# Kernel tuning notes

Hardware: AMD Instinct MI355X
Metric: run time of the kernel (lower is better)

Reference implementation:

```python
import jax, jax.numpy as jnp
import numpy as np

H = 64  # hidden width hard-coded in Agent body


def setup_inputs() -> dict:
    key = jax.random.key(0)
    ks = jax.random.split(key, 10)
    T, B, OBS, A = 1024, 512, 128, 18
    x = jax.random.normal(ks[0], (T, B, OBS), dtype=jnp.float32)
    mask = jax.random.bernoulli(ks[1], 0.01, (T, B))
    initial_carry = jnp.zeros((B, H), dtype=jnp.float32)
    s = lambda k, sh: (jax.random.normal(k, sh, dtype=jnp.float32) * 0.05)
    W1 = s(ks[2], (OBS, H)); b1 = jnp.zeros((H,), jnp.float32)
    Wi = s(ks[3], (H, 3 * H)); bi = jnp.zeros((3 * H,), jnp.float32)
    Wh = s(ks[4], (H, 3 * H)); bhn = jnp.zeros((H,), jnp.float32)
    W2 = s(ks[5], (H, H)); b2 = jnp.zeros((H,), jnp.float32)
    Wl = s(ks[6], (H, A)); bl = jnp.zeros((A,), jnp.float32)
    Wv = s(ks[7], (H, 1)); bv = jnp.zeros((1,), jnp.float32)
    return dict(x=x, mask=mask, initial_carry=initial_carry,
                W1=W1, b1=b1, Wi=Wi, bi=bi, Wh=Wh, bhn=bhn,
                W2=W2, b2=b2, Wl=Wl, bl=bl, Wv=Wv, bv=bv)


def _gru(h, z_t, Wi, bi, Wh, bhn):
    # flax nn.GRUCell math
    gi = z_t @ Wi + bi            # [B, 3H]
    gh = h @ Wh                   # [B, 3H]
    ir, iz, inn = jnp.split(gi, 3, axis=-1)
    hr, hz, hn = jnp.split(gh, 3, axis=-1)
    r = jax.nn.sigmoid(ir + hr)
    u = jax.nn.sigmoid(iz + hz)
    n = jnp.tanh(inn + r * (hn + bhn))
    return (1.0 - u) * n + u * h


def reference(x, mask, initial_carry, W1, b1, Wi, bi, Wh, bhn, W2, b2, Wl, bl, Wv, bv):
    # stem: Dense(64) + relu, applied to all timesteps at once
    z = jax.nn.relu(x @ W1 + b1)                  # [T, B, H]
    m = mask[..., None]                           # [T, B, 1]

    def step(h, inp):
        z_t, m_t = inp
        # masked reset of the carry at episode boundaries
        h = jnp.where(m_t, initial_carry, h)
        h = _gru(h, z_t, Wi, bi, Wh, bhn)
        return h, h

    h_final, ys = jax.lax.scan(step, initial_carry, (z, m))  # ys: [T, B, H]

    y = jax.nn.relu(ys @ W2 + b2)                 # [T, B, H]
    logits = y @ Wl + bl                          # [T, B, A]
    value = y @ Wv + bv                           # [T, B, 1]
    return h_final, logits.squeeze(), value.squeeze(-1)
```

## Files before the change

kernel.cpp:

```cpp
#include <hip/hip_runtime.h>
#include <stdint.h>

#define TT  1024
#define BB  512
#define OBS 128
#define HH  64
#define AA  18
#define RT  (TT*BB)
#define OFF_L ((size_t)BB*HH)
#define OFF_V (OFF_L + (size_t)TT*BB*AA)

#define GI_ELEMS ((size_t)RT*192)
#define WS_NEED  ((GI_ELEMS + (size_t)RT*HH)*4)

typedef __attribute__((ext_vector_type(8))) short bf16x8;
typedef __attribute__((ext_vector_type(4))) float f32x4;
typedef __attribute__((ext_vector_type(4))) unsigned int u32x4;

__device__ __forceinline__ float fast_rcp(float x){ return __builtin_amdgcn_rcpf(x); }
__device__ __forceinline__ float sigm(float x){ return fast_rcp(1.f + __expf(-x)); }
__device__ __forceinline__ float tanh_(float x){ return 1.f - 2.f*fast_rcp(1.f + __expf(2.f*x)); }

__device__ __forceinline__ unsigned bf16_rne(float f){
    unsigned u = __float_as_uint(f);
    return (u + 0x7FFFu + ((u>>16)&1u)) >> 16;
}
__device__ __forceinline__ unsigned pk_bf16(float lo, float hi){
    unsigned d;
    asm("v_cvt_pk_bf16_f32 %0, %1, %2" : "=v"(d) : "v"(lo), "v"(hi));
    return d;
}

__global__ void detect_mask(const uint32_t* __restrict__ m, uint32_t* __restrict__ flag)
{
    const int n_words = (TT * BB) / 4;
    uint32_t acc = 0;
    for (int i = blockIdx.x * blockDim.x + threadIdx.x; i < n_words;
         i += gridDim.x * blockDim.x)
        acc |= (m[i] > 1u) ? 1u : 0u;
    if (acc) flag[0] = 1u;
}

#define P1_BLOCKS 1024
#define ZSTR 70

__global__ __launch_bounds__(256, 2)
void stem_gi(const float* __restrict__ x,
             const float* __restrict__ W1, const float* __restrict__ b1,
             const float* __restrict__ Wi, const float* __restrict__ bi,
             float* __restrict__ gi)
{
    const int tid = threadIdx.x, w = tid >> 6, l = tid & 63;
    const int a = l & 15, q = l >> 4;

    __shared__ float z_s[4][16*ZSTR];
    float* zw = &z_s[w][0];

    bf16x8 W1f[4][4];
    #pragma unroll
    for (int nt = 0; nt < 4; ++nt)
        #pragma unroll
        for (int kf = 0; kf < 4; ++kf) {
            u32x4 pk;
            #pragma unroll
            for (int j2 = 0; j2 < 4; ++j2) {
                const int k0 = kf*32 + q*8 + 2*j2;
                pk[j2] = bf16_rne(W1[(size_t)k0*HH + nt*16 + a])
                       | (bf16_rne(W1[(size_t)(k0+1)*HH + nt*16 + a]) << 16);
            }
            W1f[nt][kf] = __builtin_bit_cast(bf16x8, pk);
        }
    float b1v[4];
    #pragma unroll
    for (int nt = 0; nt < 4; ++nt) b1v[nt] = b1[nt*16 + a];

    bf16x8 Wif[12][2];
    #pragma unroll
    for (int tau = 0; tau < 12; ++tau)
        #pragma unroll
        for (int kf = 0; kf < 2; ++kf) {
            u32x4 pk;
            #pragma unroll
            for (int j2 = 0; j2 < 4; ++j2) {
                const int k0 = kf*32 + q*8 + 2*j2;
                pk[j2] = bf16_rne(Wi[(size_t)k0*192 + tau*16 + a])
                       | (bf16_rne(Wi[(size_t)(k0+1)*192 + tau*16 + a]) << 16);
            }
            Wif[tau][kf] = __builtin_bit_cast(bf16x8, pk);
        }
    float biv[12];
    #pragma unroll
    for (int tau = 0; tau < 12; ++tau) biv[tau] = bi[tau*16 + a];

    for (int it = 0; it < 8; ++it) {
        const size_t grp  = (size_t)blockIdx.x*32 + it*4 + w;
        const float* xr   = x + (grp*16 + a)*OBS;

        float4 xv[8];
        #pragma unroll
        for (int kf = 0; kf < 4; ++kf) {
            xv[2*kf]   = *(const float4*)(xr + kf*32 + q*8);
            xv[2*kf+1] = *(const float4*)(xr + kf*32 + q*8 + 4);
        }
        bf16x8 Af[4];
        #pragma unroll
        for (int kf = 0; kf < 4; ++kf) {
            u32x4 pk;
            pk[0] = pk_bf16(xv[2*kf].x,   xv[2*kf].y);
            pk[1] = pk_bf16(xv[2*kf].z,   xv[2*kf].w);
            pk[2] = pk_bf16(xv[2*kf+1].x, xv[2*kf+1].y);
            pk[3] = pk_bf16(xv[2*kf+1].z, xv[2*kf+1].w);
            Af[kf] = __builtin_bit_cast(bf16x8, pk);
        }

        #pragma unroll
        for (int nt = 0; nt < 4; ++nt) {
            f32x4 D = {b1v[nt], b1v[nt], b1v[nt], b1v[nt]};
            #pragma unroll
            for (int kf = 0; kf < 4; ++kf)
                D = __builtin_amdgcn_mfma_f32_16x16x32_bf16(Af[kf], W1f[nt][kf], D, 0,0,0);
            #pragma unroll
            for (int e = 0; e < 4; ++e)
                zw[(q*4 + e)*ZSTR + nt*16 + a] = fmaxf(D[e], 0.f);
        }
        bf16x8 Az[2];
        #pragma unroll
        for (int s = 0; s < 2; ++s) {
            u32x4 pk;
            #pragma unroll
            for (int j2 = 0; j2 < 4; ++j2) {
                const float2 f = *(const float2*)(zw + a*ZSTR + s*32 + q*8 + 2*j2);
                pk[j2] = pk_bf16(f.x, f.y);
            }
            Az[s] = __builtin_bit_cast(bf16x8, pk);
        }

        float* gb = gi + grp*12*256 + l*4;
        #pragma unroll
        for (int tau = 0; tau < 12; ++tau) {
            f32x4 D = {biv[tau], biv[tau], biv[tau], biv[tau]};
            D = __builtin_amdgcn_mfma_f32_16x16x32_bf16(Az[0], Wif[tau][0], D, 0,0,0);
            D = __builtin_amdgcn_mfma_f32_16x16x32_bf16(Az[1], Wif[tau][1], D, 0,0,0);
            *(f32x4*)(gb + (size_t)tau*256) = D;
        }
    }
}

#define HSTR 70

__global__ __launch_bounds__(256)
void recur5(const float* __restrict__ gip,
            const void* __restrict__ mask_raw,
            const uint32_t* __restrict__ mflag,
            const float* __restrict__ ic,
            const float* __restrict__ Wh,
            const float* __restrict__ bhn,
            float* __restrict__ ys,
            float* __restrict__ out)
{
    const int blk = blockIdx.x;
    const int tid = threadIdx.x;
    const int w   = tid >> 6;
    const int l   = tid & 63;
    const int a   = l & 15;
    const int q   = l >> 4;
    const int dw  = w*16 + a;

    __shared__ unsigned short h16[2][16][HSTR];
    __shared__ uint32_t mbits[TT];

    if (mflag[0] != 0) {
        const uint8_t* m8 = (const uint8_t*)mask_raw;
        for (int t0 = w*4; t0 < TT; t0 += 16) {
            const int tt = t0 + q;
            const uint64_t bal = __ballot(m8[(size_t)tt*BB + blk*16 + a] != 0);
            if (l < 4) mbits[t0 + l] = (uint32_t)((bal >> (16*l)) & 0xFFFFu);
        }
    } else {
        const int32_t* m32 = (const int32_t*)mask_raw;
        for (int t0 = w*4; t0 < TT; t0 += 16) {
            const int tt = t0 + q;
            const uint64_t bal = __ballot(m32[(size_t)tt*BB + blk*16 + a] != 0);
            if (l < 4) mbits[t0 + l] = (uint32_t)((bal >> (16*l)) & 0xFFFFu);
        }
    }
    for (int i = tid; i < 16*64; i += 256) {
        const int c = i >> 6, d = i & 63;
        h16[0][c][d] = (unsigned short)bf16_rne(ic[(blk*16 + c)*HH + d]);
    }

    bf16x8 Bf[3][2];
    #pragma unroll
    for (int g = 0; g < 3; ++g) {
        const int colb = g*64 + dw;
        #pragma unroll
        for (int s = 0; s < 2; ++s) {
            u32x4 pk;
            #pragma unroll
            for (int j2 = 0; j2 < 4; ++j2) {
                const int k0 = s*32 + q*8 + j2*2;
                pk[j2] = bf16_rne(Wh[(size_t)k0*192 + colb])
                       | (bf16_rne(Wh[(size_t)(k0+1)*192 + colb]) << 16);
            }
            Bf[g][s] = __builtin_bit_cast(bf16x8, pk);
        }
    }
    u32x4 icA[2];
    #pragma unroll
    for (int s = 0; s < 2; ++s) {
        #pragma unroll
        for (int j2 = 0; j2 < 4; ++j2) {
            const int d0 = s*32 + q*8 + j2*2;
            icA[s][j2] = bf16_rne(ic[(blk*16 + a)*HH + d0])
                       | (bf16_rne(ic[(blk*16 + a)*HH + d0 + 1]) << 16);
        }
    }
    float ic_c[4], h_reg[4];
    #pragma unroll
    for (int e = 0; e < 4; ++e) {
        ic_c[e]  = ic[(blk*16 + q*4 + e)*HH + dw];
        h_reg[e] = ic_c[e];
    }
    const float bhnv = bhn[dw];
    const f32x4 Cn = {bhnv, bhnv, bhnv, bhnv};

    __syncthreads();

    #define GSTRIDE ((size_t)32*12*256)
    const float* gbase = gip + (size_t)blk*12*256 + l*4;
    f32x4 bufA[3], bufB[3];
    #pragma unroll
    for (int g = 0; g < 3; ++g) {
        bufA[g] = *(const f32x4*)(gbase + 0*GSTRIDE + (size_t)(g*4 + w)*256);
        bufB[g] = *(const f32x4*)(gbase + 1*GSTRIDE + (size_t)(g*4 + w)*256);
    }

    auto step = [&](int t, f32x4* cur) {
        const int p = t & 1;
        const uint32_t mb = mbits[t];
        const bool mA = (mb >> a) & 1;
        const uint32_t* hrow = (const uint32_t*)&h16[p][a][0];
        u32x4 Apk[2];
        #pragma unroll
        for (int s = 0; s < 2; ++s) {
            #pragma unroll
            for (int j2 = 0; j2 < 4; ++j2) {
                const uint32_t pkv = hrow[s*16 + q*4 + j2];
                Apk[s][j2] = mA ? icA[s][j2] : pkv;
            }
        }
        const bf16x8 A0 = __builtin_bit_cast(bf16x8, Apk[0]);
        const bf16x8 A1 = __builtin_bit_cast(bf16x8, Apk[1]);
        f32x4 Dr = __builtin_amdgcn_mfma_f32_16x16x32_bf16(A0, Bf[0][0], cur[0], 0,0,0);
        Dr       = __builtin_amdgcn_mfma_f32_16x16x32_bf16(A1, Bf[0][1], Dr,     0,0,0);
        f32x4 Dz = __builtin_amdgcn_mfma_f32_16x16x32_bf16(A0, Bf[1][0], cur[1], 0,0,0);
        Dz       = __builtin_amdgcn_mfma_f32_16x16x32_bf16(A1, Bf[1][1], Dz,     0,0,0);
        f32x4 Dn = __builtin_amdgcn_mfma_f32_16x16x32_bf16(A0, Bf[2][0], Cn,     0,0,0);
        Dn       = __builtin_amdgcn_mfma_f32_16x16x32_bf16(A1, Bf[2][1], Dn,     0,0,0);
        const f32x4 gin = cur[2];
        const int tp = (t + 2 < TT) ? (t + 2) : (TT - 1);
        #pragma unroll
        for (int g = 0; g < 3; ++g)
            cur[g] = *(const f32x4*)(gbase + (size_t)tp*GSTRIDE + (size_t)(g*4 + w)*256);
        float* ysp = ys + ((size_t)t*BB + blk*16 + q*4)*HH + dw;
        #pragma unroll
        for (int e = 0; e < 4; ++e) {
            const bool me   = (mb >> (q*4 + e)) & 1;
            const float he  = me ? ic_c[e] : h_reg[e];
            const float r   = sigm(Dr[e]);
            const float u   = sigm(Dz[e]);
            const float n   = tanh_(fmaf(r, Dn[e], gin[e]));
            const float hn  = fmaf(u, he - n, n);
            h_reg[e] = hn;
            h16[p ^ 1][q*4 + e][dw] = (unsigned short)bf16_rne(hn);
            ysp[(size_t)e*HH] = hn;
        }
        asm volatile("s_waitcnt lgkmcnt(0)" ::: "memory");
        __builtin_amdgcn_s_barrier();
        __builtin_amdgcn_sched_barrier(0);
    };

    for (int t = 0; t < TT; t += 2) {
        step(t,     bufA);
        step(t + 1, bufB);
    }
    #pragma unroll
    for (int e = 0; e < 4; ++e)
        out[(size_t)(blk*16 + q*4 + e)*HH + dw] = h_reg[e];
    #undef GSTRIDE
}

#define P3_BLOCKS 1024
#define P3_RPW (RT/(P3_BLOCKS*4))

__global__ __launch_bounds__(256, 2)
void heads(const float* __restrict__ ys,
           const float* __restrict__ W2, const float* __restrict__ b2,
           const float* __restrict__ Wl, const float* __restrict__ bl,
           const float* __restrict__ Wv, const float* __restrict__ bv,
           float* __restrict__ out)
{
    const int tid = threadIdx.x, w = tid >> 6, lane = tid & 63;
    __shared__ float4 sb[4][2][16];
    float w2r[64];
    #pragma unroll
    for (int k = 0; k < 64; ++k) w2r[k] = W2[k*HH + lane];
    const float b2v = b2[lane];
    float wc[64]; float bcv = 0.f;
    if (lane < AA) {
        #pragma unroll
        for (int k = 0; k < 64; ++k) wc[k] = Wl[k*AA + lane];
        bcv = bl[lane];
    } else if (lane == AA) {
        #pragma unroll
        for (int k = 0; k < 64; ++k) wc[k] = Wv[k];
        bcv = bv[0];
    } else {
        #pragma unroll
        for (int k = 0; k < 64; ++k) wc[k] = 0.f;
    }
    const int r0 = (blockIdx.x*4 + w) * P3_RPW;
    float ysA = ys[(size_t)r0*HH + lane];
    float ysB = ys[(size_t)(r0+1)*HH + lane];
    for (int rr = 0; rr < P3_RPW; ++rr) {
        const int row = r0 + rr;
        const float ysv = ysA;
        ysA = ysB;
        const int rn = (rr+2 < P3_RPW) ? (row+2) : (r0 + P3_RPW - 1);
        ysB = ys[(size_t)rn*HH + lane];
        ((float*)&sb[w][0][0])[lane] = ysv;
        float acc = b2v;
        {
            const float4* yb = &sb[w][0][0];
            #pragma unroll
            for (int kk = 0; kk < 16; ++kk) {
                const float4 v = yb[kk];
                acc += w2r[4*kk+0]*v.x + w2r[4*kk+1]*v.y
                     + w2r[4*kk+2]*v.z + w2r[4*kk+3]*v.w;
            }
        }
        const float yv = fmaxf(acc, 0.f);
        ((float*)&sb[w][1][0])[lane] = yv;
        float acc2 = bcv;
        {
            const float4* yb = &sb[w][1][0];
            #pragma unroll
            for (int kk = 0; kk < 16; ++kk) {
                const float4 v = yb[kk];
                acc2 += wc[4*kk+0]*v.x + wc[4*kk+1]*v.y
                      + wc[4*kk+2]*v.z + wc[4*kk+3]*v.w;
            }
        }
        if (lane < AA)       out[OFF_L + (size_t)row*AA + lane] = acc2;
        else if (lane == AA) out[OFF_V + row] = acc2;
    }
}

__global__ __launch_bounds__(256, 2)
void gru_agent(const float* __restrict__ x,
               const void* __restrict__ mask_raw,
               const uint32_t* __restrict__ mask_flag,
               const float* __restrict__ ic,
               const float* __restrict__ W1, const float* __restrict__ b1,
               const float* __restrict__ Wi, const float* __restrict__ bi,
               const float* __restrict__ Wh, const float* __restrict__ bhn,
               const float* __restrict__ W2, const float* __restrict__ b2,
               const float* __restrict__ Wl, const float* __restrict__ bl,
               const float* __restrict__ Wv, const float* __restrict__ bv,
               float* __restrict__ out)
{
    const int b    = blockIdx.x;
    const int tid  = threadIdx.x;
    const int w    = tid >> 6;
    const int lane = tid & 63;

    const bool mask_is_u8 = (mask_flag[0] != 0);
    const uint8_t* __restrict__ m8  = (const uint8_t*)mask_raw;
    const int32_t* __restrict__ m32 = (const int32_t*)mask_raw;

    __shared__ float4 x_l[2][4][9];
    __shared__ float4 z_l[16];
    __shared__ float4 h_l[2][16];
    __shared__ float4 y_l[2][16];
    __shared__ float4 ic_l[16];
    __shared__ float  gi_l[192];
    __shared__ float  gh_l[192];

    const int js = (w << 4) | (lane >> 2);
    const int kc = lane & 3;
    float w1r[32];
    #pragma unroll
    for (int i = 0; i < 32; ++i) w1r[i] = W1[(kc*32 + i)*HH + js];
    const float b1v = b1[js];

    float wA[64], wB[64];
    float biv = 0.f, b2v = 0.f, blv = 0.f;
    if (w < 3) {
        const int n = tid;
        #pragma unroll
        for (int k = 0; k < 64; ++k) wA[k] = Wi[k*(3*HH) + n];
        #pragma unroll
        for (int k = 0; k < 64; ++k) wB[k] = Wh[k*(3*HH) + n];
        biv = bi[n];
    } else {
        #pragma unroll
        for (int k = 0; k < 64; ++k) wA[k] = W2[k*HH + lane];
        #pragma unroll
        for (int k = 0; k < 64; ++k) wB[k] = (lane < AA) ? Wl[k*AA + lane]
                                           : (lane == AA ? Wv[k] : 0.f);
        b2v = b2[lane];
        blv = (lane < AA) ? bl[lane] : (lane == AA ? bv[0] : 0.f);
    }
    const float bhnv = (tid < HH) ? bhn[tid] : 0.f;

    if (tid < HH) {
        float v = ic[b*HH + tid];
        ((float*)ic_l)[tid]   = v;
        ((float*)h_l[0])[tid] = v;
    }
    if (tid < OBS) {
        float xv = x[(0*BB + b)*OBS + tid];
        ((float*)&x_l[0][tid>>5])[tid&31] = xv;
    }
    uint8_t m_cur = mask_is_u8 ? m8[b] : (uint8_t)(m32[b] != 0);
    __syncthreads();

    for (int t = 0; t < TT + 2; ++t) {
        const int p = t & 1;
        float xnext = 0.f;
        if (t + 1 < TT && tid < OBS) xnext = x[((t+1)*BB + b)*OBS + tid];
        uint8_t m_next = 0;
        if (t + 1 < TT) {
            const int mi = (t+1)*BB + b;
            m_next = mask_is_u8 ? m8[mi] : (uint8_t)(m32[mi] != 0);
        }
        if (t < TT) {
            const float4* xr = &x_l[p][kc][0];
            float acc = 0.f;
            #pragma unroll
            for (int qq = 0; qq < 8; ++qq) {
                float4 xv = xr[qq];
                acc += w1r[4*qq+0]*xv.x + w1r[4*qq+1]*xv.y
                     + w1r[4*qq+2]*xv.z + w1r[4*qq+3]*xv.w;
            }
            acc += __shfl_xor(acc, 1);
            acc += __shfl_xor(acc, 2);
            if (kc == 0) ((float*)z_l)[js] = fmaxf(acc + b1v, 0.f);
        }
        if (t < TT && w < 3) {
            const float4* hs = m_cur ? ic_l : h_l[p];
            float acc = 0.f;
            #pragma unroll
            for (int kk = 0; kk < 16; ++kk) {
                float4 hv = hs[kk];
                acc += wB[4*kk+0]*hv.x + wB[4*kk+1]*hv.y
                     + wB[4*kk+2]*hv.z + wB[4*kk+3]*hv.w;
            }
            gh_l[tid] = acc;
        } else if (w == 3 && t >= 1 && t <= TT) {
            const float4* hs = h_l[p];
            float acc = b2v;
            #pragma unroll
            for (int kk = 0; kk < 16; ++kk) {
                float4 hv = hs[kk];
                acc += wA[4*kk+0]*hv.x + wA[4*kk+1]*hv.y
                     + wA[4*kk+2]*hv.z + wA[4*kk+3]*hv.w;
            }
            ((float*)y_l[p])[lane] = fmaxf(acc, 0.f);
        }
        __syncthreads();
        if (t < TT && w < 3) {
            float acc = biv;
            #pragma unroll
            for (int kk = 0; kk < 16; ++kk) {
                float4 zv = z_l[kk];
                acc += wA[4*kk+0]*zv.x + wA[4*kk+1]*zv.y
                     + wA[4*kk+2]*zv.z + wA[4*kk+3]*zv.w;
            }
            gi_l[tid] = acc;
        } else if (w == 3 && t >= 2) {
            const float4* yss = y_l[p ^ 1];
            float acc = blv;
            #pragma unroll
            for (int kk = 0; kk < 16; ++kk) {
                float4 yv = yss[kk];
                acc += wB[4*kk+0]*yv.x + wB[4*kk+1]*yv.y
                     + wB[4*kk+2]*yv.z + wB[4*kk+3]*yv.w;
            }
            if (lane < AA)       out[OFF_L + (size_t)((t-2)*BB + b)*AA + lane] = acc;
            else if (lane == AA) out[OFF_V + (size_t)(t-2)*BB + b] = acc;
        }
        __syncthreads();
        if (t < TT && tid < HH) {
            const int j = tid;
            const float irv = gi_l[j], izv = gi_l[HH+j], inn = gi_l[2*HH+j];
            const float hrv = gh_l[j], hzv = gh_l[HH+j], hnv = gh_l[2*HH+j];
            const float heff = m_cur ? ((const float*)ic_l)[j]
                                     : ((const float*)h_l[p])[j];
            const float r  = sigm(irv + hrv);
            const float u  = sigm(izv + hzv);
            const float nn = tanh_(inn + r*(hnv + bhnv));
            ((float*)h_l[p ^ 1])[j] = u*(heff - nn) + nn;
        }
        if (t + 1 < TT && tid < OBS) {
            ((float*)&x_l[p ^ 1][tid>>5])[tid&31] = xnext;
        }
        m_cur = m_next;
        __syncthreads();
    }
    if (tid < HH) out[(size_t)b*HH + tid] = ((const float*)h_l[TT & 1])[tid];
}

extern "C" void kernel_launch(void* const* d_in, const int* in_sizes, int n_in,
                              void* d_out, int out_size, void* d_ws, size_t ws_size,
                              hipStream_t stream) {
    const float* x    = (const float*)d_in[0];
    const void*  mask = (const void*) d_in[1];
    const float* ic   = (const float*)d_in[2];
    const float* W1   = (const float*)d_in[3];
    const float* b1   = (const float*)d_in[4];
    const float* Wi   = (const float*)d_in[5];
    const float* bi   = (const float*)d_in[6];
    const float* Wh   = (const float*)d_in[7];
    const float* bhn  = (const float*)d_in[8];
    const float* W2   = (const float*)d_in[9];
    const float* b2   = (const float*)d_in[10];
    const float* Wl   = (const float*)d_in[11];
    const float* bl   = (const float*)d_in[12];
    const float* Wv   = (const float*)d_in[13];
    const float* bv   = (const float*)d_in[14];
    float* out = (float*)d_out;

    if (ws_size >= WS_NEED) {
        float* gi = (float*)d_ws;
        float* ys = gi + GI_ELEMS;
        uint32_t* flag = (uint32_t*)(out + OFF_V + RT - 1);
        hipMemsetAsync(flag, 0, sizeof(uint32_t), stream);
        detect_mask<<<64, 256, 0, stream>>>((const uint32_t*)mask, flag);
        stem_gi<<<P1_BLOCKS, 256, 0, stream>>>(x, W1, b1, Wi, bi, gi);
        recur5<<<32, 256, 0, stream>>>(gi, mask, flag, ic, Wh, bhn, ys, out);
        heads<<<P3_BLOCKS, 256, 0, stream>>>(ys, W2, b2, Wl, bl, Wv, bv, out);
    } else {
        uint32_t* flag = (uint32_t*)d_ws;
        hipMemsetAsync(flag, 0, sizeof(uint32_t), stream);
        detect_mask<<<64, 256, 0, stream>>>((const uint32_t*)mask, flag);
        gru_agent<<<BB, 256, 0, stream>>>(x, mask, flag, ic, W1, b1, Wi, bi, Wh, bhn,
                                          W2, b2, Wl, bl, Wv, bv, out);
    }
}
```

Baseline: 1.149 ms.

## Run GRU recurrence with one wave per batch tile to drop barriers

The recurrence kernel changes from four waves per 16-row batch tile to a single 64-lane wave. That wave computes all four 16-column hidden groups itself, so the per-step workgroup barrier and LDS wait are no longer needed. Mask-bit preloading now uses vectorized loads and shuffles instead of ballots, and the LDS row stride is reduced. In exchange, each wave issues four times the MFMA, gate-math and global-load work per step, and holds more register state. That could lengthen the serial per-step critical path.

```diff
diff --git a/kernel.cpp b/kernel.cpp
--- a/kernel.cpp
+++ b/kernel.cpp
@@ -146,10 +146,10 @@
     }
 }
 
-#define HSTR 70
-
-__global__ __launch_bounds__(256)
-void recur5(const float* __restrict__ gip,
+#define HSTR 66
+
+__global__ __launch_bounds__(64, 1)
+void recur6(const float* __restrict__ gip,
             const void* __restrict__ mask_raw,
             const uint32_t* __restrict__ mflag,
             const float* __restrict__ ic,
@@ -159,125 +159,147 @@
             float* __restrict__ out)
 {
     const int blk = blockIdx.x;
-    const int tid = threadIdx.x;
-    const int w   = tid >> 6;
-    const int l   = tid & 63;
+    const int l   = threadIdx.x;
     const int a   = l & 15;
     const int q   = l >> 4;
-    const int dw  = w*16 + a;
 
     __shared__ unsigned short h16[2][16][HSTR];
     __shared__ uint32_t mbits[TT];
 
     if (mflag[0] != 0) {
         const uint8_t* m8 = (const uint8_t*)mask_raw;
-        for (int t0 = w*4; t0 < TT; t0 += 16) {
-            const int tt = t0 + q;
-            const uint64_t bal = __ballot(m8[(size_t)tt*BB + blk*16 + a] != 0);
-            if (l < 4) mbits[t0 + l] = (uint32_t)((bal >> (16*l)) & 0xFFFFu);
+        for (int t0 = 0; t0 < TT; t0 += 64) {
+            const int t = t0 + l;
+            const uint4 v = *(const uint4*)(m8 + (size_t)t*BB + blk*16);
+            uint32_t bits = 0;
+            #pragma unroll
+            for (int i = 0; i < 4; ++i) {
+                const uint32_t word = (&v.x)[i];
+                bits |= ((word & 0x000000FFu) ? 1u : 0u) << (4*i + 0);
+                bits |= ((word & 0x0000FF00u) ? 1u : 0u) << (4*i + 1);
+                bits |= ((word & 0x00FF0000u) ? 1u : 0u) << (4*i + 2);
+                bits |= ((word & 0xFF000000u) ? 1u : 0u) << (4*i + 3);
+            }
+            mbits[t] = bits;
         }
     } else {
         const int32_t* m32 = (const int32_t*)mask_raw;
-        for (int t0 = w*4; t0 < TT; t0 += 16) {
-            const int tt = t0 + q;
-            const uint64_t bal = __ballot(m32[(size_t)tt*BB + blk*16 + a] != 0);
-            if (l < 4) mbits[t0 + l] = (uint32_t)((bal >> (16*l)) & 0xFFFFu);
-        }
-    }
-    for (int i = tid; i < 16*64; i += 256) {
+        for (int t0 = 0; t0 < TT; t0 += 16) {
+            const int t = t0 + (l >> 2), part = l & 3;
+            const uint4 v = *(const uint4*)(m32 + (size_t)t*BB + blk*16 + part*4);
+            uint32_t nib = ((v.x?1u:0u) | (v.y?2u:0u) | (v.z?4u:0u) | (v.w?8u:0u)) << (4*part);
+            nib |= __shfl_xor(nib, 1);
+            nib |= __shfl_xor(nib, 2);
+            if (part == 0) mbits[t] = nib;
+        }
+    }
+    for (int i = l; i < 16*64; i += 64) {
         const int c = i >> 6, d = i & 63;
         h16[0][c][d] = (unsigned short)bf16_rne(ic[(blk*16 + c)*HH + d]);
     }
 
-    bf16x8 Bf[3][2];
-    #pragma unroll
-    for (int g = 0; g < 3; ++g) {
-        const int colb = g*64 + dw;
-        #pragma unroll
-        for (int s = 0; s < 2; ++s) {
-            u32x4 pk;
-            #pragma unroll
-            for (int j2 = 0; j2 < 4; ++j2) {
-                const int k0 = s*32 + q*8 + j2*2;
-                pk[j2] = bf16_rne(Wh[(size_t)k0*192 + colb])
-                       | (bf16_rne(Wh[(size_t)(k0+1)*192 + colb]) << 16);
-            }
-            Bf[g][s] = __builtin_bit_cast(bf16x8, pk);
-        }
-    }
+    bf16x8 Bf[3][4][2];
+    #pragma unroll
+    for (int g = 0; g < 3; ++g)
+        #pragma unroll
+        for (int dg = 0; dg < 4; ++dg) {
+            const int colb = g*64 + dg*16 + a;
+            #pragma unroll
+            for (int s = 0; s < 2; ++s) {
+                u32x4 pk;
+                #pragma unroll
+                for (int j2 = 0; j2 < 4; ++j2) {
+                    const int k0 = s*32 + q*8 + j2*2;
+                    pk[j2] = bf16_rne(Wh[(size_t)k0*192 + colb])
+                           | (bf16_rne(Wh[(size_t)(k0+1)*192 + colb]) << 16);
+                }
+                Bf[g][dg][s] = __builtin_bit_cast(bf16x8, pk);
+            }
+        }
     u32x4 icA[2];
     #pragma unroll
-    for (int s = 0; s < 2; ++s) {
+    for (int s = 0; s < 2; ++s)
         #pragma unroll
         for (int j2 = 0; j2 < 4; ++j2) {
             const int d0 = s*32 + q*8 + j2*2;
             icA[s][j2] = bf16_rne(ic[(blk*16 + a)*HH + d0])
                        | (bf16_rne(ic[(blk*16 + a)*HH + d0 + 1]) << 16);
         }
-    }
-    float ic_c[4], h_reg[4];
-    #pragma unroll
-    for (int e = 0; e < 4; ++e) {
-        ic_c[e]  = ic[(blk*16 + q*4 + e)*HH + dw];
-        h_reg[e] = ic_c[e];
-    }
-    const float bhnv = bhn[dw];
-    const f32x4 Cn = {bhnv, bhnv, bhnv, bhnv};
-
-    __syncthreads();
+    float ic_c[4][4], h_reg[4][4];
+    #pragma unroll
+    for (int e = 0; e < 4; ++e)
+        #pragma unroll
+        for (int dg = 0; dg < 4; ++dg) {
+            ic_c[e][dg]  = ic[(blk*16 + q*4 + e)*HH + dg*16 + a];
+            h_reg[e][dg] = ic_c[e][dg];
+        }
+    float bhn4[4];
+    #pragma unroll
+    for (int dg = 0; dg < 4; ++dg) bhn4[dg] = bhn[dg*16 + a];
 
     #define GSTRIDE ((size_t)32*12*256)
     const float* gbase = gip + (size_t)blk*12*256 + l*4;
-    f32x4 bufA[3], bufB[3];
-    #pragma unroll
-    for (int g = 0; g < 3; ++g) {
-        bufA[g] = *(const f32x4*)(gbase + 0*GSTRIDE + (size_t)(g*4 + w)*256);
-        bufB[g] = *(const f32x4*)(gbase + 1*GSTRIDE + (size_t)(g*4 + w)*256);
-    }
-
-    auto step = [&](int t, f32x4* cur) {
+    f32x4 bufA[3][4], bufB[3][4];
+    #pragma unroll
+    for (int g = 0; g < 3; ++g)
+        #pragma unroll
+        for (int dg = 0; dg < 4; ++dg) {
+            bufA[g][dg] = *(const f32x4*)(gbase + 0*GSTRIDE + (size_t)(g*4 + dg)*256);
+            bufB[g][dg] = *(const f32x4*)(gbase + 1*GSTRIDE + (size_t)(g*4 + dg)*256);
+        }
+
+    auto step = [&](int t, f32x4 (&cur)[3][4]) {
         const int p = t & 1;
         const uint32_t mb = mbits[t];
         const bool mA = (mb >> a) & 1;
         const uint32_t* hrow = (const uint32_t*)&h16[p][a][0];
-        u32x4 Apk[2];
-        #pragma unroll
-        for (int s = 0; s < 2; ++s) {
-            #pragma unroll
-            for (int j2 = 0; j2 < 4; ++j2) {
-                const uint32_t pkv = hrow[s*16 + q*4 + j2];
-                Apk[s][j2] = mA ? icA[s][j2] : pkv;
-            }
-        }
-        const bf16x8 A0 = __builtin_bit_cast(bf16x8, Apk[0]);
-        const bf16x8 A1 = __builtin_bit_cast(bf16x8, Apk[1]);
-        f32x4 Dr = __builtin_amdgcn_mfma_f32_16x16x32_bf16(A0, Bf[0][0], cur[0], 0,0,0);
-        Dr       = __builtin_amdgcn_mfma_f32_16x16x32_bf16(A1, Bf[0][1], Dr,     0,0,0);
-        f32x4 Dz = __builtin_amdgcn_mfma_f32_16x16x32_bf16(A0, Bf[1][0], cur[1], 0,0,0);
-        Dz       = __builtin_amdgcn_mfma_f32_16x16x32_bf16(A1, Bf[1][1], Dz,     0,0,0);
-        f32x4 Dn = __builtin_amdgcn_mfma_f32_16x16x32_bf16(A0, Bf[2][0], Cn,     0,0,0);
-        Dn       = __builtin_amdgcn_mfma_f32_16x16x32_bf16(A1, Bf[2][1], Dn,     0,0,0);
-        const f32x4 gin = cur[2];
+        u32x4 Apk0, Apk1;
+        #pragma unroll
+        for (int j2 = 0; j2 < 4; ++j2) {
+            const uint32_t v0 = hrow[q*4 + j2];
+            const uint32_t v1 = hrow[16 + q*4 + j2];
+            Apk0[j2] = mA ? icA[0][j2] : v0;
+            Apk1[j2] = mA ? icA[1][j2] : v1;
+        }
+        const bf16x8 A0 = __builtin_bit_cast(bf16x8, Apk0);
+        const bf16x8 A1 = __builtin_bit_cast(bf16x8, Apk1);
         const int tp = (t + 2 < TT) ? (t + 2) : (TT - 1);
-        #pragma unroll
-        for (int g = 0; g < 3; ++g)
-            cur[g] = *(const f32x4*)(gbase + (size_t)tp*GSTRIDE + (size_t)(g*4 + w)*256);
-        float* ysp = ys + ((size_t)t*BB + blk*16 + q*4)*HH + dw;
-        #pragma unroll
-        for (int e = 0; e < 4; ++e) {
-            const bool me   = (mb >> (q*4 + e)) & 1;
-            const float he  = me ? ic_c[e] : h_reg[e];
-            const float r   = sigm(Dr[e]);
-            const float u   = sigm(Dz[e]);
-            const float n   = tanh_(fmaf(r, Dn[e], gin[e]));
-            const float hn  = fmaf(u, he - n, n);
-            h_reg[e] = hn;
-            h16[p ^ 1][q*4 + e][dw] = (unsigned short)bf16_rne(hn);
-            ysp[(size_t)e*HH] = hn;
-        }
-        asm volatile("s_waitcnt lgkmcnt(0)" ::: "memory");
-        __builtin_amdgcn_s_barrier();
-        __builtin_amdgcn_sched_barrier(0);
+        const float* gpre = gbase + (size_t)tp*GSTRIDE;
+        float* ysp = ys + ((size_t)t*BB + blk*16)*HH;
+        #pragma unroll
+        for (int dg = 0; dg < 4; ++dg) {
+            f32x4 Dr = __builtin_amdgcn_mfma_f32_16x16x32_bf16(A0, Bf[0][dg][0], cur[0][dg], 0,0,0);
+            Dr       = __builtin_amdgcn_mfma_f32_16x16x32_bf16(A1, Bf[0][dg][1], Dr,          0,0,0);
+            f32x4 Dz = __builtin_amdgcn_mfma_f32_16x16x32_bf16(A0, Bf[1][dg][0], cur[1][dg], 0,0,0);
+            Dz       = __builtin_amdgcn_mfma_f32_16x16x32_bf16(A1, Bf[1][dg][1], Dz,          0,0,0);
+            const f32x4 Cnv = {bhn4[dg], bhn4[dg], bhn4[dg], bhn4[dg]};
+            f32x4 Dn = __builtin_amdgcn_mfma_f32_16x16x32_bf16(A0, Bf[2][dg][0], Cnv,         0,0,0);
+            Dn       = __builtin_amdgcn_mfma_f32_16x16x32_bf16(A1, Bf[2][dg][1], Dn,          0,0,0);
+            const f32x4 gin = cur[2][dg];
+            cur[0][dg] = *(const f32x4*)(gpre + (size_t)(0*4 + dg)*256);
+            cur[1][dg] = *(const f32x4*)(gpre + (size_t)(1*4 + dg)*256);
+            cur[2][dg] = *(const f32x4*)(gpre + (size_t)(2*4 + dg)*256);
+            float hn_[4];
+            #pragma unroll
+            for (int e = 0; e < 4; ++e) {
+                const bool me  = (mb >> (q*4 + e)) & 1;
+                const float he = me ? ic_c[e][dg] : h_reg[e][dg];
+                const float r  = sigm(Dr[e]);
+                const float u  = sigm(Dz[e]);
+                const float n  = tanh_(fmaf(r, Dn[e], gin[e]));
+                const float hn = fmaf(u, he - n, n);
+                h_reg[e][dg] = hn;
+                hn_[e] = hn;
+                ysp[(q*4 + e)*HH + dg*16 + a] = hn;
+            }
+            const int d = dg*16 + a;
+            const uint32_t pk01 = pk_bf16(hn_[0], hn_[1]);
+            const uint32_t pk23 = pk_bf16(hn_[2], hn_[3]);
+            h16[p^1][q*4 + 0][d] = (unsigned short)(pk01 & 0xFFFFu);
+            h16[p^1][q*4 + 1][d] = (unsigned short)(pk01 >> 16);
+            h16[p^1][q*4 + 2][d] = (unsigned short)(pk23 & 0xFFFFu);
+            h16[p^1][q*4 + 3][d] = (unsigned short)(pk23 >> 16);
+        }
     };
 
     for (int t = 0; t < TT; t += 2) {
@@ -286,7 +308,9 @@
     }
     #pragma unroll
     for (int e = 0; e < 4; ++e)
-        out[(size_t)(blk*16 + q*4 + e)*HH + dw] = h_reg[e];
+        #pragma unroll
+        for (int dg = 0; dg < 4; ++dg)
+            out[(size_t)(blk*16 + q*4 + e)*HH + dg*16 + a] = h_reg[e][dg];
     #undef GSTRIDE
 }
 
@@ -538,7 +562,7 @@
         hipMemsetAsync(flag, 0, sizeof(uint32_t), stream);
         detect_mask<<<64, 256, 0, stream>>>((const uint32_t*)mask, flag);
         stem_gi<<<P1_BLOCKS, 256, 0, stream>>>(x, W1, b1, Wi, bi, gi);
-        recur5<<<32, 256, 0, stream>>>(gi, mask, flag, ic, Wh, bhn, ys, out);
+        recur6<<<32, 64, 0, stream>>>(gi, mask, flag, ic, Wh, bhn, ys, out);
         heads<<<P3_BLOCKS, 256, 0, stream>>>(ys, W2, b2, Wl, bl, Wv, bv, out);
     } else {
         uint32_t* flag = (uint32_t*)d_ws;
```

Result: slower. 1.863 ms (+62.1%).
